# Performance work log

Measured on AMD Instinct MI355X. Metric: run time of the kernel, lower is better.

Reference implementation:

```python
import jax, jax.numpy as jnp
import numpy as np

E = 8          # num_global_experts (experts['count_per_node'])
D = 1024       # model_dim
H = 2048       # expert hidden_size
TOP_K = 2      # gate_type['k']


def setup_inputs() -> dict:
    key = jax.random.key(0)
    k_x, k_g, k_w1, k_w2 = jax.random.split(key, 4)
    B, S = 4, 2048
    inp = {
        "input": jax.random.normal(k_x, (B, S, D), dtype=jnp.float32),
        "Wg": jax.random.normal(k_g, (D, E), dtype=jnp.float32) * 0.02,
        "W1": jax.random.normal(k_w1, (E, D, H), dtype=jnp.float32) * 0.02,
        "b1": jnp.zeros((E, H), dtype=jnp.float32),
        "W2": jax.random.normal(k_w2, (E, H, D), dtype=jnp.float32) * 0.02,
        "b2": jnp.zeros((E, D), dtype=jnp.float32),
    }
    return inp


def reference(input, Wg, W1, b1, W2, b2):
    # ---- router: top-k softmax gating, gate weights normalized over top-k ----
    logits = jnp.einsum("bsd,de->bse", input, Wg)            # [B,S,E]
    probs = jax.nn.softmax(logits, axis=-1)                   # [B,S,E]
    top_vals, top_idx = jax.lax.top_k(probs, TOP_K)           # [B,S,K]
    top_vals = top_vals / jnp.sum(top_vals, axis=-1, keepdims=True)
    onehot = jax.nn.one_hot(top_idx, E, dtype=input.dtype)    # [B,S,K,E]
    mask = jnp.sum(onehot, axis=2)                            # [B,S,E] 0/1 dispatch mask (indices)
    scores = jnp.sum(onehot * top_vals[..., None], axis=2)    # [B,S,E] combine weights

    # ---- dense masked dispatch: repeat input per expert, mask non-routed tokens ----
    xm = input[None] * jnp.moveaxis(mask, -1, 0)[..., None]   # [E,B,S,D]

    # ---- per-expert 2-layer MLP (LinearExperts) ----
    h = jnp.einsum("ebsd,edh->ebsh", xm, W1) + b1[:, None, None, :]
    h = jax.nn.relu(h)                                        # [E,B,S,H]
    y = jnp.einsum("ebsh,ehd->ebsd", h, W2) + b2[:, None, None, :]

    # ---- weighted combine: sum_e expert_out * gate score ----
    out = jnp.sum(y * jnp.moveaxis(scores, -1, 0)[..., None], axis=0)  # [B,S,D]
    return out
```

## Files before the change

kernel.cpp:

```cpp
#include <hip/hip_runtime.h>
#include <hip/hip_bf16.h>

typedef __bf16 bf16x8 __attribute__((ext_vector_type(8)));
typedef __bf16 bf16x4 __attribute__((ext_vector_type(4)));
typedef float  f32x4  __attribute__((ext_vector_type(4)));

#define T_TOK    8192
#define D_DIM    1024
#define H_DIM    2048
#define E_NUM    8
#define MAX_MB   136
#define MAX_ROWS 17408

#define OFF_MBTOT   512
#define OFF_MB2E    1024
#define OFF_MBROW0  2048
#define OFF_TOPKE   4096
#define OFF_TOPKS   69632
#define OFF_TOK     135168
#define OFF_ROWIDX  204800
#define OFF_XB      (1u<<20)
#define OFF_W1T     (18u*1024*1024)
#define OFF_W2T     (50u*1024*1024)
#define OFF_HBUF    (82u*1024*1024)
#define OFF_YBUF    OFF_XB

__device__ __forceinline__ void gload_lds16(const void* g, void* l) {
    __builtin_amdgcn_global_load_lds(
        (const __attribute__((address_space(1))) void*)g,
        (__attribute__((address_space(3))) void*)l, 16, 0, 0);
}

__global__ __launch_bounds__(256) void k_router_cvt(
    const float* __restrict__ x, const float* __restrict__ Wg,
    __bf16* __restrict__ xb, int* __restrict__ topk_e, float* __restrict__ topk_s)
{
    const int tid = threadIdx.x;
    const int wave = tid >> 6, lane = tid & 63;
    const int t = blockIdx.x * 4 + wave;
    const float* xr = x + (size_t)t * D_DIM;
    __bf16* xbr = xb + (size_t)t * D_DIM;

    float acc[E_NUM];
#pragma unroll
    for (int e = 0; e < E_NUM; ++e) acc[e] = 0.f;

#pragma unroll
    for (int j = 0; j < 4; ++j) {
        const int d0 = lane * 4 + j * 256;
        float4 xv = *(const float4*)(xr + d0);
        bf16x4 o = { (__bf16)xv.x, (__bf16)xv.y, (__bf16)xv.z, (__bf16)xv.w };
        *(bf16x4*)(xbr + d0) = o;
        const float* xvf = (const float*)&xv;
#pragma unroll
        for (int u = 0; u < 4; ++u) {
            float4 wlo = *(const float4*)(Wg + (size_t)(d0 + u) * E_NUM);
            float4 whi = *(const float4*)(Wg + (size_t)(d0 + u) * E_NUM + 4);
            float xd = xvf[u];
            acc[0] += xd * wlo.x; acc[1] += xd * wlo.y;
            acc[2] += xd * wlo.z; acc[3] += xd * wlo.w;
            acc[4] += xd * whi.x; acc[5] += xd * whi.y;
            acc[6] += xd * whi.z; acc[7] += xd * whi.w;
        }
    }
#pragma unroll
    for (int off = 32; off >= 1; off >>= 1)
#pragma unroll
        for (int e = 0; e < E_NUM; ++e) acc[e] += __shfl_xor(acc[e], off, 64);

    if (lane == 0) {
        int e0 = 0; float v0 = acc[0];
#pragma unroll
        for (int e = 1; e < E_NUM; ++e) if (acc[e] > v0) { v0 = acc[e]; e0 = e; }
        int e1 = -1; float v1 = -1e30f;
#pragma unroll
        for (int e = 0; e < E_NUM; ++e) if (e != e0 && acc[e] > v1) { v1 = acc[e]; e1 = e; }
        float s0 = 1.f / (1.f + __expf(v1 - v0));
        float s1 = 1.f - s0;
        topk_e[t*2+0] = e0; topk_e[t*2+1] = e1;
        topk_s[t*2+0] = s0; topk_s[t*2+1] = s1;
    }
}

#define SORT_T 256
__global__ __launch_bounds__(512) void k_sort(
    const int* __restrict__ topk_e,
    int* __restrict__ mbTot, int* __restrict__ mb2e, int* __restrict__ mbrow0,
    int* __restrict__ tok, int* __restrict__ rowidx)
{
    __shared__ int lcnt[E_NUM][SORT_T];
    __shared__ int base[E_NUM];
    __shared__ int etot[E_NUM];
    const int tid = threadIdx.x;

    if (tid < SORT_T) {
#pragma unroll
        for (int e = 0; e < E_NUM; ++e) lcnt[e][tid] = 0;
    }
    __syncthreads();

    if (tid < SORT_T) {
        const int4* p = (const int4*)(topk_e + tid * 64);
#pragma unroll
        for (int i = 0; i < 16; ++i) {
            int4 v = p[i];
            lcnt[v.x][tid]++; lcnt[v.y][tid]++; lcnt[v.z][tid]++; lcnt[v.w][tid]++;
        }
    }
    __syncthreads();

    {
        const int w = tid >> 6, l = tid & 63;
        int v0 = lcnt[w][l*4+0], v1 = lcnt[w][l*4+1], v2 = lcnt[w][l*4+2], v3 = lcnt[w][l*4+3];
        int s = v0 + v1 + v2 + v3;
        int inc = s;
#pragma unroll
        for (int off = 1; off < 64; off <<= 1) {
            int o = __shfl_up(inc, off, 64);
            if (l >= off) inc += o;
        }
        int exc = inc - s;
        lcnt[w][l*4+0] = exc;
        lcnt[w][l*4+1] = exc + v0;
        lcnt[w][l*4+2] = exc + v0 + v1;
        lcnt[w][l*4+3] = exc + v0 + v1 + v2;
        if (l == 63) etot[w] = inc;
    }
    __syncthreads();

    if (tid == 0) {
        int row = 0, mb = 0;
        for (int e = 0; e < E_NUM; ++e) {
            base[e] = row;
            int nb = (etot[e] + 127) >> 7;
            for (int b = 0; b < nb; ++b) { mb2e[mb] = e; mbrow0[mb] = row + b*128; ++mb; }
            row += nb * 128;
        }
        mbTot[0] = mb;
    }
    __syncthreads();

    if (tid < SORT_T) {
#pragma unroll
        for (int e = 0; e < E_NUM; ++e) lcnt[e][tid] += base[e];
        const int4* p = (const int4*)(topk_e + tid * 64);
#pragma unroll
        for (int i = 0; i < 16; ++i) {
            int4 v = p[i];
            int j0 = tid * 64 + i * 4;
            int r;
            r = lcnt[v.x][tid]++; tok[r] = (j0+0) >> 1; rowidx[j0+0] = r;
            r = lcnt[v.y][tid]++; tok[r] = (j0+1) >> 1; rowidx[j0+1] = r;
            r = lcnt[v.z][tid]++; tok[r] = (j0+2) >> 1; rowidx[j0+2] = r;
            r = lcnt[v.w][tid]++; tok[r] = (j0+3) >> 1; rowidx[j0+3] = r;
        }
    }
}

__global__ __launch_bounds__(256) void k_transpose(
    const float* __restrict__ in, __bf16* __restrict__ out, int R, int C)
{
    __shared__ float tile[64][65];
    const int e = blockIdx.z;
    const float* inp = in + (size_t)e * R * C;
    __bf16* outp = out + (size_t)e * R * C;
    const int r0 = blockIdx.x * 64, c0 = blockIdx.y * 64;
    const int c = threadIdx.x & 63, rr = threadIdx.x >> 6;
#pragma unroll
    for (int i = 0; i < 16; ++i) {
        int r = rr + i * 4;
        tile[r][c] = inp[(size_t)(r0 + r) * C + c0 + c];
    }
    __syncthreads();
#pragma unroll
    for (int i = 0; i < 16; ++i) {
        int cc = rr + i * 4;
        outp[(size_t)(c0 + cc) * R + r0 + c] = (__bf16)tile[c][cc];
    }
}


__global__ __launch_bounds__(256) void k_gemm1(
    const __bf16* __restrict__ xb, const __bf16* __restrict__ W1T,
    const float* __restrict__ b1, const int* __restrict__ tok,
    const int* __restrict__ mb2e, const int* __restrict__ mbrow0,
    const int* __restrict__ mbTot, __bf16* __restrict__ hbuf)
{
    const int id   = blockIdx.x;
    const int xcd  = id & 7;
    const int j    = id >> 3;
    const int nblk = j & 15;
    const int mb   = (j >> 4) * 8 + xcd;
    if (mb >= *mbTot) return;
    const int e    = mb2e[mb];
    const int row0 = mbrow0[mb];
    const int n0   = nblk * 128;

    __shared__ __align__(16) char smem[32768];

    const int tid = threadIdx.x;
    const int w = tid >> 6, l = tid & 63;
    const int lrow  = l >> 3;
    const int chunk = (l & 7) ^ lrow;

    const __bf16* Wb = W1T + (size_t)e * (size_t)(H_DIM * D_DIM);
    const __bf16* gA[4]; const __bf16* gB[4];
#pragma unroll
    for (int jj = 0; jj < 4; ++jj) {
        int rr = w*32 + jj*8 + lrow;
        gA[jj] = xb + (size_t)tok[row0 + rr] * D_DIM + chunk * 8;
        gB[jj] = Wb + (size_t)(n0 + rr) * D_DIM + chunk * 8;
    }
    char* ldsA = smem + w*4096 + l*16;
    char* ldsB = smem + 16384 + w*4096 + l*16;

    const int r = l & 15, q = l >> 4;
    const int wm = w & 1, wn = w >> 1;
    const int r7 = r & 7;

    f32x4 acc[4][4];
#pragma unroll
    for (int mi = 0; mi < 4; ++mi)
#pragma unroll
        for (int ni = 0; ni < 4; ++ni) acc[mi][ni] = (f32x4){0.f, 0.f, 0.f, 0.f};

    for (int k0 = 0; k0 < D_DIM; k0 += 64) {
#pragma unroll
        for (int jj = 0; jj < 4; ++jj) gload_lds16(gA[jj] + k0, ldsA + jj*1024);
#pragma unroll
        for (int jj = 0; jj < 4; ++jj) gload_lds16(gB[jj] + k0, ldsB + jj*1024);
        __syncthreads();

#pragma unroll
        for (int s = 0; s < 2; ++s) {
            const int cx = ((s*4 + q) ^ r7) * 16;
            bf16x8 av[4], bv[4];
#pragma unroll
            for (int mi = 0; mi < 4; ++mi)
                av[mi] = *(const bf16x8*)(smem + (wm*64 + mi*16 + r) * 128 + cx);
#pragma unroll
            for (int ni = 0; ni < 4; ++ni)
                bv[ni] = *(const bf16x8*)(smem + 16384 + (wn*64 + ni*16 + r) * 128 + cx);
#pragma unroll
            for (int mi = 0; mi < 4; ++mi)
#pragma unroll
                for (int ni = 0; ni < 4; ++ni)
                    acc[mi][ni] = __builtin_amdgcn_mfma_f32_16x16x32_bf16(av[mi], bv[ni], acc[mi][ni], 0, 0, 0);
        }
        __syncthreads();
    }

    const float* b1e = b1 + (size_t)e * H_DIM;
    float bb[4];
#pragma unroll
    for (int ni = 0; ni < 4; ++ni) bb[ni] = b1e[n0 + wn*64 + ni*16 + r];
#pragma unroll
    for (int mi = 0; mi < 4; ++mi)
#pragma unroll
        for (int reg = 0; reg < 4; ++reg) {
            int m = wm*64 + mi*16 + q*4 + reg;
            __bf16* hrow = hbuf + (size_t)(row0 + m) * H_DIM + n0 + wn*64;
#pragma unroll
            for (int ni = 0; ni < 4; ++ni) {
                float v = acc[mi][ni][reg] + bb[ni];
                hrow[ni*16 + r] = (__bf16)fmaxf(v, 0.f);
            }
        }
}

__global__ __launch_bounds__(256) void k_gemm2(
    const __bf16* __restrict__ hbuf, const __bf16* __restrict__ W2T,
    const float* __restrict__ b2, const int* __restrict__ mb2e,
    const int* __restrict__ mbrow0, const int* __restrict__ mbTot,
    __bf16* __restrict__ ybuf)
{
    const int id   = blockIdx.x;
    const int xcd  = id & 7;
    const int j    = id >> 3;
    const int nblk = j & 7;
    const int mb   = (j >> 3) * 8 + xcd;
    if (mb >= *mbTot) return;
    const int e    = mb2e[mb];
    const int row0 = mbrow0[mb];
    const int n0   = nblk * 128;

    __shared__ __align__(16) char smem[32768];

    const int tid = threadIdx.x;
    const int w = tid >> 6, l = tid & 63;
    const int lrow  = l >> 3;
    const int chunk = (l & 7) ^ lrow;

    const __bf16* Wb = W2T + (size_t)e * (size_t)(D_DIM * H_DIM);
    const __bf16* gA[4]; const __bf16* gB[4];
#pragma unroll
    for (int jj = 0; jj < 4; ++jj) {
        int rr = w*32 + jj*8 + lrow;
        gA[jj] = hbuf + (size_t)(row0 + rr) * H_DIM + chunk * 8;
        gB[jj] = Wb + (size_t)(n0 + rr) * H_DIM + chunk * 8;
    }
    char* ldsA = smem + w*4096 + l*16;
    char* ldsB = smem + 16384 + w*4096 + l*16;

    const int r = l & 15, q = l >> 4;
    const int wm = w & 1, wn = w >> 1;
    const int r7 = r & 7;

    f32x4 acc[4][4];
#pragma unroll
    for (int mi = 0; mi < 4; ++mi)
#pragma unroll
        for (int ni = 0; ni < 4; ++ni) acc[mi][ni] = (f32x4){0.f, 0.f, 0.f, 0.f};

    for (int k0 = 0; k0 < H_DIM; k0 += 64) {
#pragma unroll
        for (int jj = 0; jj < 4; ++jj) gload_lds16(gA[jj] + k0, ldsA + jj*1024);
#pragma unroll
        for (int jj = 0; jj < 4; ++jj) gload_lds16(gB[jj] + k0, ldsB + jj*1024);
        __syncthreads();

#pragma unroll
        for (int s = 0; s < 2; ++s) {
            const int cx = ((s*4 + q) ^ r7) * 16;
            bf16x8 av[4], bv[4];
#pragma unroll
            for (int mi = 0; mi < 4; ++mi)
                av[mi] = *(const bf16x8*)(smem + (wm*64 + mi*16 + r) * 128 + cx);
#pragma unroll
            for (int ni = 0; ni < 4; ++ni)
                bv[ni] = *(const bf16x8*)(smem + 16384 + (wn*64 + ni*16 + r) * 128 + cx);
#pragma unroll
            for (int mi = 0; mi < 4; ++mi)
#pragma unroll
                for (int ni = 0; ni < 4; ++ni)
                    acc[mi][ni] = __builtin_amdgcn_mfma_f32_16x16x32_bf16(av[mi], bv[ni], acc[mi][ni], 0, 0, 0);
        }
        __syncthreads();
    }

    const float* b2e = b2 + (size_t)e * D_DIM;
    float bb[4];
#pragma unroll
    for (int ni = 0; ni < 4; ++ni) bb[ni] = b2e[n0 + wn*64 + ni*16 + r];
#pragma unroll
    for (int mi = 0; mi < 4; ++mi)
#pragma unroll
        for (int reg = 0; reg < 4; ++reg) {
            int row = row0 + wm*64 + mi*16 + q*4 + reg;
            __bf16* yrow = ybuf + (size_t)row * D_DIM + n0 + wn*64;
#pragma unroll
            for (int ni = 0; ni < 4; ++ni)
                yrow[ni*16 + r] = (__bf16)(acc[mi][ni][reg] + bb[ni]);
        }
}

__global__ __launch_bounds__(256) void k_combine(
    const __bf16* __restrict__ ybuf, const int* __restrict__ rowidx,
    const float* __restrict__ topk_s, float* __restrict__ out)
{
    const int t = blockIdx.x;
    const int d0 = threadIdx.x * 4;
    const int r0 = rowidx[t*2+0], r1 = rowidx[t*2+1];
    const float s0 = topk_s[t*2+0], s1 = topk_s[t*2+1];
    bf16x4 y0 = *(const bf16x4*)(ybuf + (size_t)r0 * D_DIM + d0);
    bf16x4 y1 = *(const bf16x4*)(ybuf + (size_t)r1 * D_DIM + d0);
    float4 o;
    o.x = s0 * (float)y0[0] + s1 * (float)y1[0];
    o.y = s0 * (float)y0[1] + s1 * (float)y1[1];
    o.z = s0 * (float)y0[2] + s1 * (float)y1[2];
    o.w = s0 * (float)y0[3] + s1 * (float)y1[3];
    *(float4*)(out + (size_t)t * D_DIM + d0) = o;
}

extern "C" void kernel_launch(void* const* d_in, const int* in_sizes, int n_in,
                              void* d_out, int out_size, void* d_ws, size_t ws_size,
                              hipStream_t stream) {
    const float* x  = (const float*)d_in[0];
    const float* Wg = (const float*)d_in[1];
    const float* W1 = (const float*)d_in[2];
    const float* b1 = (const float*)d_in[3];
    const float* W2 = (const float*)d_in[4];
    const float* b2 = (const float*)d_in[5];
    float* out = (float*)d_out;
    char* ws = (char*)d_ws;

    int*   mbTot  = (int*)  (ws + OFF_MBTOT);
    int*   mb2e   = (int*)  (ws + OFF_MB2E);
    int*   mbrow0 = (int*)  (ws + OFF_MBROW0);
    int*   topk_e = (int*)  (ws + OFF_TOPKE);
    float* topk_s = (float*)(ws + OFF_TOPKS);
    int*   tok    = (int*)  (ws + OFF_TOK);
    int*   rowidx = (int*)  (ws + OFF_ROWIDX);
    __bf16* xb   = (__bf16*)(ws + OFF_XB);
    __bf16* W1T  = (__bf16*)(ws + OFF_W1T);
    __bf16* W2T  = (__bf16*)(ws + OFF_W2T);
    __bf16* hbuf = (__bf16*)(ws + OFF_HBUF);
    __bf16* ybuf = (__bf16*)(ws + OFF_YBUF);

    hipMemsetAsync(ws + OFF_TOK, 0, MAX_ROWS * sizeof(int), stream);

    k_router_cvt<<<T_TOK/4, 256, 0, stream>>>(x, Wg, xb, topk_e, topk_s);
    k_sort      <<<1, 512, 0, stream>>>(topk_e, mbTot, mb2e, mbrow0, tok, rowidx);
    k_transpose <<<dim3(D_DIM/64, H_DIM/64, E_NUM), 256, 0, stream>>>(W1, W1T, D_DIM, H_DIM);
    k_transpose <<<dim3(H_DIM/64, D_DIM/64, E_NUM), 256, 0, stream>>>(W2, W2T, H_DIM, D_DIM);

    k_gemm1<<<MAX_MB * (H_DIM/128), 256, 0, stream>>>(xb, W1T, b1, tok, mb2e, mbrow0, mbTot, hbuf);
    k_gemm2<<<MAX_MB * (D_DIM/128), 256, 0, stream>>>(hbuf, W2T, b2, mb2e, mbrow0, mbTot, ybuf);
    k_combine<<<T_TOK, 256, 0, stream>>>(ybuf, rowidx, topk_s, out);
}
```

Before: 452.8 us.

## Halve GEMM M-tile to 64 with 2-wave blocks, fuse transposes, stage Wg in LDS

The expert GEMMs now use 64x128 tiles with 128-thread blocks, doubling the number of row blocks per expert. This improves load balance and occupancy, at the cost of reloading more B-tile data per FLOP. The router copies the gate matrix into padded shared memory instead of doing strided global reads. The two weight transposes are merged into one launch, and the tok memset moves into the sort kernel, removing launches. Together these cut launch overhead and underutilised tail blocks, while adding more weight traffic in the GEMMs.

```diff
diff --git a/kernel.cpp b/kernel.cpp
--- a/kernel.cpp
+++ b/kernel.cpp
@@ -9,12 +9,12 @@
 #define D_DIM    1024
 #define H_DIM    2048
 #define E_NUM    8
-#define MAX_MB   136
+#define MAX_MB   272
 #define MAX_ROWS 17408
 
 #define OFF_MBTOT   512
 #define OFF_MB2E    1024
-#define OFF_MBROW0  2048
+#define OFF_MBROW0  2560
 #define OFF_TOPKE   4096
 #define OFF_TOPKS   69632
 #define OFF_TOK     135168
@@ -35,7 +35,15 @@
     const float* __restrict__ x, const float* __restrict__ Wg,
     __bf16* __restrict__ xb, int* __restrict__ topk_e, float* __restrict__ topk_s)
 {
+    __shared__ float wgP[D_DIM * 9];
     const int tid = threadIdx.x;
+#pragma unroll
+    for (int i = 0; i < 32; ++i) {
+        int f = tid + i * 256;
+        wgP[(f >> 3) * 9 + (f & 7)] = Wg[f];
+    }
+    __syncthreads();
+
     const int wave = tid >> 6, lane = tid & 63;
     const int t = blockIdx.x * 4 + wave;
     const float* xr = x + (size_t)t * D_DIM;
@@ -45,23 +53,20 @@
 #pragma unroll
     for (int e = 0; e < E_NUM; ++e) acc[e] = 0.f;
 
+#pragma unroll
+    for (int j = 0; j < 16; ++j) {
+        const int d = j * 64 + lane;
+        const float xd = xr[d];
+        const float* wr = &wgP[d * 9];
+#pragma unroll
+        for (int e = 0; e < E_NUM; ++e) acc[e] += xd * wr[e];
+    }
 #pragma unroll
     for (int j = 0; j < 4; ++j) {
         const int d0 = lane * 4 + j * 256;
         float4 xv = *(const float4*)(xr + d0);
         bf16x4 o = { (__bf16)xv.x, (__bf16)xv.y, (__bf16)xv.z, (__bf16)xv.w };
         *(bf16x4*)(xbr + d0) = o;
-        const float* xvf = (const float*)&xv;
-#pragma unroll
-        for (int u = 0; u < 4; ++u) {
-            float4 wlo = *(const float4*)(Wg + (size_t)(d0 + u) * E_NUM);
-            float4 whi = *(const float4*)(Wg + (size_t)(d0 + u) * E_NUM + 4);
-            float xd = xvf[u];
-            acc[0] += xd * wlo.x; acc[1] += xd * wlo.y;
-            acc[2] += xd * wlo.z; acc[3] += xd * wlo.w;
-            acc[4] += xd * whi.x; acc[5] += xd * whi.y;
-            acc[6] += xd * whi.z; acc[7] += xd * whi.w;
-        }
     }
 #pragma unroll
     for (int off = 32; off >= 1; off >>= 1)
@@ -92,6 +97,8 @@
     __shared__ int base[E_NUM];
     __shared__ int etot[E_NUM];
     const int tid = threadIdx.x;
+
+    for (int i = tid; i < MAX_ROWS; i += 512) tok[i] = 0;
 
     if (tid < SORT_T) {
 #pragma unroll
@@ -133,7 +140,7 @@
         for (int e = 0; e < E_NUM; ++e) {
             base[e] = row;
             int nb = (etot[e] + 127) >> 7;
-            for (int b = 0; b < nb; ++b) { mb2e[mb] = e; mbrow0[mb] = row + b*128; ++mb; }
+            for (int b = 0; b < 2*nb; ++b) { mb2e[mb] = e; mbrow0[mb] = row + b*64; ++mb; }
             row += nb * 128;
         }
         mbTot[0] = mb;
@@ -157,14 +164,25 @@
     }
 }
 
-__global__ __launch_bounds__(256) void k_transpose(
-    const float* __restrict__ in, __bf16* __restrict__ out, int R, int C)
+__global__ __launch_bounds__(256) void k_transpose_all(
+    const float* __restrict__ W1, __bf16* __restrict__ W1T,
+    const float* __restrict__ W2, __bf16* __restrict__ W2T)
 {
     __shared__ float tile[64][65];
-    const int e = blockIdx.z;
-    const float* inp = in + (size_t)e * R * C;
-    __bf16* outp = out + (size_t)e * R * C;
-    const int r0 = blockIdx.x * 64, c0 = blockIdx.y * 64;
+    int id = blockIdx.x;
+    const float* inp; __bf16* outp; int R, C, r0, c0;
+    if (id < 4096) {
+        int e = id >> 9, tl = id & 511;
+        R = D_DIM; C = H_DIM;
+        r0 = (tl & 15) * 64; c0 = (tl >> 4) * 64;
+        inp = W1 + (size_t)e * R * C; outp = W1T + (size_t)e * R * C;
+    } else {
+        id -= 4096;
+        int e = id >> 9, tl = id & 511;
+        R = H_DIM; C = D_DIM;
+        r0 = (tl & 31) * 64; c0 = (tl >> 5) * 64;
+        inp = W2 + (size_t)e * R * C; outp = W2T + (size_t)e * R * C;
+    }
     const int c = threadIdx.x & 63, rr = threadIdx.x >> 6;
 #pragma unroll
     for (int i = 0; i < 16; ++i) {
@@ -180,7 +198,7 @@
 }
 
 
-__global__ __launch_bounds__(256) void k_gemm1(
+__global__ __launch_bounds__(128) void k_gemm1(
     const __bf16* __restrict__ xb, const __bf16* __restrict__ W1T,
     const float* __restrict__ b1, const int* __restrict__ tok,
     const int* __restrict__ mb2e, const int* __restrict__ mbrow0,
@@ -196,7 +214,7 @@
     const int row0 = mbrow0[mb];
     const int n0   = nblk * 128;
 
-    __shared__ __align__(16) char smem[32768];
+    __shared__ __align__(16) char smem[24576];
 
     const int tid = threadIdx.x;
     const int w = tid >> 6, l = tid & 63;
@@ -204,18 +222,33 @@
     const int chunk = (l & 7) ^ lrow;
 
     const __bf16* Wb = W1T + (size_t)e * (size_t)(H_DIM * D_DIM);
-    const __bf16* gA[4]; const __bf16* gB[4];
+    const __bf16* gA[2]; const __bf16* gB[4];
+#pragma unroll
+    for (int jj = 0; jj < 2; ++jj) {
+        int rr = jj*16 + w*8 + lrow;
+        gA[jj] = xb + (size_t)tok[row0 + rr] * D_DIM + chunk * 8;
+    }
+    const __bf16* gA2[2];
+#pragma unroll
+    for (int jj = 0; jj < 2; ++jj) {
+        int rr = 32 + jj*16 + w*8 + lrow;
+        gA2[jj] = xb + (size_t)tok[row0 + rr] * D_DIM + chunk * 8;
+    }
 #pragma unroll
     for (int jj = 0; jj < 4; ++jj) {
-        int rr = w*32 + jj*8 + lrow;
-        gA[jj] = xb + (size_t)tok[row0 + rr] * D_DIM + chunk * 8;
+        int rr = jj*16 + w*8 + lrow;
         gB[jj] = Wb + (size_t)(n0 + rr) * D_DIM + chunk * 8;
     }
-    char* ldsA = smem + w*4096 + l*16;
-    char* ldsB = smem + 16384 + w*4096 + l*16;
+    const __bf16* gB2[4];
+#pragma unroll
+    for (int jj = 0; jj < 4; ++jj) {
+        int rr = 64 + jj*16 + w*8 + lrow;
+        gB2[jj] = Wb + (size_t)(n0 + rr) * D_DIM + chunk * 8;
+    }
+    char* ldsA = smem + w*1024 + l*16;
+    char* ldsB = smem + 8192 + w*1024 + l*16;
 
     const int r = l & 15, q = l >> 4;
-    const int wm = w & 1, wn = w >> 1;
     const int r7 = r & 7;
 
     f32x4 acc[4][4];
@@ -226,9 +259,13 @@
 
     for (int k0 = 0; k0 < D_DIM; k0 += 64) {
 #pragma unroll
-        for (int jj = 0; jj < 4; ++jj) gload_lds16(gA[jj] + k0, ldsA + jj*1024);
-#pragma unroll
-        for (int jj = 0; jj < 4; ++jj) gload_lds16(gB[jj] + k0, ldsB + jj*1024);
+        for (int jj = 0; jj < 2; ++jj) gload_lds16(gA[jj]  + k0, ldsA + jj*2048);
+#pragma unroll
+        for (int jj = 0; jj < 2; ++jj) gload_lds16(gA2[jj] + k0, ldsA + 4096 + jj*2048);
+#pragma unroll
+        for (int jj = 0; jj < 4; ++jj) gload_lds16(gB[jj]  + k0, ldsB + jj*2048);
+#pragma unroll
+        for (int jj = 0; jj < 4; ++jj) gload_lds16(gB2[jj] + k0, ldsB + 8192 + jj*2048);
         __syncthreads();
 
 #pragma unroll
@@ -237,10 +274,10 @@
             bf16x8 av[4], bv[4];
 #pragma unroll
             for (int mi = 0; mi < 4; ++mi)
-                av[mi] = *(const bf16x8*)(smem + (wm*64 + mi*16 + r) * 128 + cx);
+                av[mi] = *(const bf16x8*)(smem + (mi*16 + r) * 128 + cx);
 #pragma unroll
             for (int ni = 0; ni < 4; ++ni)
-                bv[ni] = *(const bf16x8*)(smem + 16384 + (wn*64 + ni*16 + r) * 128 + cx);
+                bv[ni] = *(const bf16x8*)(smem + 8192 + (w*64 + ni*16 + r) * 128 + cx);
 #pragma unroll
             for (int mi = 0; mi < 4; ++mi)
 #pragma unroll
@@ -253,13 +290,13 @@
     const float* b1e = b1 + (size_t)e * H_DIM;
     float bb[4];
 #pragma unroll
-    for (int ni = 0; ni < 4; ++ni) bb[ni] = b1e[n0 + wn*64 + ni*16 + r];
+    for (int ni = 0; ni < 4; ++ni) bb[ni] = b1e[n0 + w*64 + ni*16 + r];
 #pragma unroll
     for (int mi = 0; mi < 4; ++mi)
 #pragma unroll
         for (int reg = 0; reg < 4; ++reg) {
-            int m = wm*64 + mi*16 + q*4 + reg;
-            __bf16* hrow = hbuf + (size_t)(row0 + m) * H_DIM + n0 + wn*64;
+            int m = mi*16 + q*4 + reg;
+            __bf16* hrow = hbuf + (size_t)(row0 + m) * H_DIM + n0 + w*64;
 #pragma unroll
             for (int ni = 0; ni < 4; ++ni) {
                 float v = acc[mi][ni][reg] + bb[ni];
@@ -268,7 +305,7 @@
         }
 }
 
-__global__ __launch_bounds__(256) void k_gemm2(
+__global__ __launch_bounds__(128) void k_gemm2(
     const __bf16* __restrict__ hbuf, const __bf16* __restrict__ W2T,
     const float* __restrict__ b2, const int* __restrict__ mb2e,
     const int* __restrict__ mbrow0, const int* __restrict__ mbTot,
@@ -284,7 +321,7 @@
     const int row0 = mbrow0[mb];
     const int n0   = nblk * 128;
 
-    __shared__ __align__(16) char smem[32768];
+    __shared__ __align__(16) char smem[24576];
 
     const int tid = threadIdx.x;
     const int w = tid >> 6, l = tid & 63;
@@ -292,18 +329,18 @@
     const int chunk = (l & 7) ^ lrow;
 
     const __bf16* Wb = W2T + (size_t)e * (size_t)(D_DIM * H_DIM);
-    const __bf16* gA[4]; const __bf16* gB[4];
+    const __bf16* gA[4]; const __bf16* gB[4]; const __bf16* gB2[4];
 #pragma unroll
     for (int jj = 0; jj < 4; ++jj) {
-        int rr = w*32 + jj*8 + lrow;
-        gA[jj] = hbuf + (size_t)(row0 + rr) * H_DIM + chunk * 8;
-        gB[jj] = Wb + (size_t)(n0 + rr) * H_DIM + chunk * 8;
-    }
-    char* ldsA = smem + w*4096 + l*16;
-    char* ldsB = smem + 16384 + w*4096 + l*16;
+        int rr = jj*16 + w*8 + lrow;
+        gA[jj]  = hbuf + (size_t)(row0 + rr) * H_DIM + chunk * 8;
+        gB[jj]  = Wb + (size_t)(n0 + rr) * H_DIM + chunk * 8;
+        gB2[jj] = Wb + (size_t)(n0 + 64 + rr) * H_DIM + chunk * 8;
+    }
+    char* ldsA = smem + w*1024 + l*16;
+    char* ldsB = smem + 8192 + w*1024 + l*16;
 
     const int r = l & 15, q = l >> 4;
-    const int wm = w & 1, wn = w >> 1;
     const int r7 = r & 7;
 
     f32x4 acc[4][4];
@@ -314,9 +351,13 @@
 
     for (int k0 = 0; k0 < H_DIM; k0 += 64) {
 #pragma unroll
-        for (int jj = 0; jj < 4; ++jj) gload_lds16(gA[jj] + k0, ldsA + jj*1024);
-#pragma unroll
-        for (int jj = 0; jj < 4; ++jj) gload_lds16(gB[jj] + k0, ldsB + jj*1024);
+        for (int jj = 0; jj < 2; ++jj) gload_lds16(gA[jj]   + k0, ldsA + jj*2048);
+#pragma unroll
+        for (int jj = 0; jj < 2; ++jj) gload_lds16(gA[2+jj] + k0, ldsA + 4096 + jj*2048);
+#pragma unroll
+        for (int jj = 0; jj < 4; ++jj) gload_lds16(gB[jj]  + k0, ldsB + jj*2048);
+#pragma unroll
+        for (int jj = 0; jj < 4; ++jj) gload_lds16(gB2[jj] + k0, ldsB + 8192 + jj*2048);
         __syncthreads();
 
 #pragma unroll
@@ -325,10 +366,10 @@
             bf16x8 av[4], bv[4];
 #pragma unroll
             for (int mi = 0; mi < 4; ++mi)
-                av[mi] = *(const bf16x8*)(smem + (wm*64 + mi*16 + r) * 128 + cx);
+                av[mi] = *(const bf16x8*)(smem + (mi*16 + r) * 128 + cx);
 #pragma unroll
             for (int ni = 0; ni < 4; ++ni)
-                bv[ni] = *(const bf16x8*)(smem + 16384 + (wn*64 + ni*16 + r) * 128 + cx);
+                bv[ni] = *(const bf16x8*)(smem + 8192 + (w*64 + ni*16 + r) * 128 + cx);
 #pragma unroll
             for (int mi = 0; mi < 4; ++mi)
 #pragma unroll
@@ -341,13 +382,13 @@
     const float* b2e = b2 + (size_t)e * D_DIM;
     float bb[4];
 #pragma unroll
-    for (int ni = 0; ni < 4; ++ni) bb[ni] = b2e[n0 + wn*64 + ni*16 + r];
+    for (int ni = 0; ni < 4; ++ni) bb[ni] = b2e[n0 + w*64 + ni*16 + r];
 #pragma unroll
     for (int mi = 0; mi < 4; ++mi)
 #pragma unroll
         for (int reg = 0; reg < 4; ++reg) {
-            int row = row0 + wm*64 + mi*16 + q*4 + reg;
-            __bf16* yrow = ybuf + (size_t)row * D_DIM + n0 + wn*64;
+            int row = row0 + mi*16 + q*4 + reg;
+            __bf16* yrow = ybuf + (size_t)row * D_DIM + n0 + w*64;
 #pragma unroll
             for (int ni = 0; ni < 4; ++ni)
                 yrow[ni*16 + r] = (__bf16)(acc[mi][ni][reg] + bb[ni]);
@@ -397,14 +438,11 @@
     __bf16* hbuf = (__bf16*)(ws + OFF_HBUF);
     __bf16* ybuf = (__bf16*)(ws + OFF_YBUF);
 
-    hipMemsetAsync(ws + OFF_TOK, 0, MAX_ROWS * sizeof(int), stream);
-
-    k_router_cvt<<<T_TOK/4, 256, 0, stream>>>(x, Wg, xb, topk_e, topk_s);
-    k_sort      <<<1, 512, 0, stream>>>(topk_e, mbTot, mb2e, mbrow0, tok, rowidx);
-    k_transpose <<<dim3(D_DIM/64, H_DIM/64, E_NUM), 256, 0, stream>>>(W1, W1T, D_DIM, H_DIM);
-    k_transpose <<<dim3(H_DIM/64, D_DIM/64, E_NUM), 256, 0, stream>>>(W2, W2T, H_DIM, D_DIM);
-
-    k_gemm1<<<MAX_MB * (H_DIM/128), 256, 0, stream>>>(xb, W1T, b1, tok, mb2e, mbrow0, mbTot, hbuf);
-    k_gemm2<<<MAX_MB * (D_DIM/128), 256, 0, stream>>>(hbuf, W2T, b2, mb2e, mbrow0, mbTot, ybuf);
+    k_router_cvt  <<<T_TOK/4, 256, 0, stream>>>(x, Wg, xb, topk_e, topk_s);
+    k_sort        <<<1, 512, 0, stream>>>(topk_e, mbTot, mb2e, mbrow0, tok, rowidx);
+    k_transpose_all<<<8192, 256, 0, stream>>>(W1, W1T, W2, W2T);
+
+    k_gemm1<<<MAX_MB * (H_DIM/128), 128, 0, stream>>>(xb, W1T, b1, tok, mb2e, mbrow0, mbTot, hbuf);
+    k_gemm2<<<MAX_MB * (D_DIM/128), 128, 0, stream>>>(hbuf, W2T, b2, mb2e, mbrow0, mbTot, ybuf);
     k_combine<<<T_TOK, 256, 0, stream>>>(ybuf, rowidx, topk_s, out);
 }
```

Measured after the change: 451.8 us. No clear change (-0.2%).
